# Performance work log

Measured on AMD Instinct MI355X. Metric: run time of the kernel, lower is better.

Reference implementation:

```python
import jax, jax.numpy as jnp
import numpy as np

N = 100000
E = 1600000
IN_DIM = 165
HID = 128
OUT_H = 64  # hidden_dim // 2

def setup_inputs() -> dict:
    key = jax.random.key(0)
    ks = jax.random.split(key, 8)
    x = jax.random.normal(ks[0], (N, IN_DIM), dtype=jnp.float32)
    edge_index = jax.random.randint(ks[1], (2, E), 0, N, dtype=jnp.int64)
    s1 = 1.0 / np.sqrt(IN_DIM)
    s2 = 1.0 / np.sqrt(HID)
    s3 = 1.0 / np.sqrt(OUT_H)
    return {
        "x": x,
        "edge_index": edge_index,
        "W1": jax.random.normal(ks[2], (IN_DIM, HID), dtype=jnp.float32) * s1,
        "b1": jnp.zeros((HID,), jnp.float32),
        "Wg": jax.random.normal(ks[3], (HID, OUT_H), dtype=jnp.float32) * s2,
        "a_src": jax.random.normal(ks[4], (OUT_H,), dtype=jnp.float32) * s3,
        "a_dst": jax.random.normal(ks[5], (OUT_H,), dtype=jnp.float32) * s3,
        "bg": jnp.zeros((OUT_H,), jnp.float32),
        "Wfc": jax.random.normal(ks[6], (OUT_H, 2), dtype=jnp.float32) * s3,
        "bfc": jnp.zeros((2,), jnp.float32),
    }

def _add_self_loops(edge_index, n):
    loops = jnp.arange(n, dtype=edge_index.dtype)
    row = jnp.concatenate([edge_index[0], loops])
    col = jnpp_concat = jnp.concatenate([edge_index[1], loops])
    return row, col

def _gcn_layer(x, row, col, W, b, n):
    deg = jax.ops.segment_sum(jnp.ones_like(col, dtype=x.dtype), col, num_segments=n)
    dinv = jnp.where(deg > 0, jax.lax.rsqrt(deg), 0.0)
    h = x @ W                                   # [N, HID]
    msg = h[row] * (dinv[row] * dinv[col])[:, None]  # [E+N, HID]
    return jax.ops.segment_sum(msg, col, num_segments=n) + b

def _gat_layer(x, row, col, W, a_src, a_dst, b, n):
    # single-head GATConv with self-loops, LeakyReLU(0.2), segment softmax over dst
    h = x @ W                                   # [N, OUT_H]
    e = jax.nn.leaky_relu((h @ a_src)[row] + (h @ a_dst)[col], negative_slope=0.2)
    m = jax.ops.segment_max(e, col, num_segments=n)
    ex = jnp.exp(e - m[col])
    s = jax.ops.segment_sum(ex, col, num_segments=n)
    alpha = ex / s[col]                         # every node has a self-loop => s > 0
    out = jax.ops.segment_sum(alpha[:, None] * h[row], col, num_segments=n)
    return out + b

def reference(x, edge_index, W1, b1, Wg, a_src, a_dst, bg, Wfc, bfc):
    n = x.shape[0]
    row, col = _add_self_loops(edge_index, n)
    h = jax.nn.relu(_gcn_layer(x, row, col, W1, b1, n))
    h = jax.nn.relu(_gat_layer(h, row, col, Wg, a_src, a_dst, bg, n))
    return h @ Wfc + bfc
```

## Files before the change

### kernel.cpp

```cpp
#include <hip/hip_runtime.h>
#include <math.h>

#define NSL 0.2f
#define IN_DIM 165
#define HID 128
#define OUT_H 64
#define NCB_MAX 512
#define EPB 4096

typedef __attribute__((ext_vector_type(8))) short bf16x8;
typedef __attribute__((ext_vector_type(4))) float f32x4;

__device__ inline unsigned pack_bf16(float a, float b) {
    unsigned ua = __float_as_uint(a);
    ua += 0x7FFFu + ((ua >> 16) & 1u);
    unsigned ub = __float_as_uint(b);
    ub += 0x7FFFu + ((ub >> 16) & 1u);
    return (ua >> 16) | (ub & 0xFFFF0000u);
}

__device__ __host__ inline int pcol(int i) {
    int j = i >> 1, odd = i & 1;
    return 32 * (j >> 4) + (j & 15) + 16 * odd;
}

__global__ __launch_bounds__(256) void chist(const int* __restrict__ coli, int E,
                                             int* __restrict__ ghist, int ncb) {
    __shared__ int h[NCB_MAX];
    for (int i = threadIdx.x; i < ncb; i += 256) h[i] = 0;
    __syncthreads();
    int e0 = blockIdx.x * EPB;
    int e1 = min(e0 + EPB, E);
    for (int e = e0 + threadIdx.x; e < e1; e += 256)
        atomicAdd(&h[coli[e] >> 8], 1);
    __syncthreads();
    for (int i = threadIdx.x; i < ncb; i += 256)
        if (h[i]) atomicAdd(&ghist[i], h[i]);
}

__global__ __launch_bounds__(NCB_MAX) void cscan(const int* __restrict__ ghist,
                                                 int* __restrict__ cstart,
                                                 int* __restrict__ gcursor,
                                                 int ncb, int E) {
    __shared__ int tmp[NCB_MAX];
    int tid = threadIdx.x;
    int v = (tid < ncb) ? ghist[tid] : 0;
    tmp[tid] = v;
    __syncthreads();
    for (int off = 1; off < NCB_MAX; off <<= 1) {
        int t = (tid >= off) ? tmp[tid - off] : 0;
        __syncthreads();
        tmp[tid] += t;
        __syncthreads();
    }
    if (tid < ncb) {
        int excl = tmp[tid] - v;
        cstart[tid] = excl;
        gcursor[tid] = excl;
    }
    if (tid == ncb - 1) cstart[ncb] = E;
}

__global__ __launch_bounds__(256) void pass1_scatter(const int* __restrict__ rowi,
                                                     const int* __restrict__ coli, int E,
                                                     int* __restrict__ gcursor,
                                                     unsigned* __restrict__ ebuf, int ncb) {
    __shared__ int hist[NCB_MAX];
    __shared__ int base[NCB_MAX];
    int e0 = blockIdx.x * EPB;
    int e1 = min(e0 + EPB, E);
    for (int i = threadIdx.x; i < ncb; i += 256) hist[i] = 0;
    __syncthreads();
    for (int e = e0 + threadIdx.x; e < e1; e += 256)
        atomicAdd(&hist[coli[e] >> 8], 1);
    __syncthreads();
    for (int i = threadIdx.x; i < ncb; i += 256) {
        int h = hist[i];
        base[i] = h ? atomicAdd(&gcursor[i], h) : 0;
        hist[i] = 0;
    }
    __syncthreads();
    for (int e = e0 + threadIdx.x; e < e1; e += 256) {
        int c = coli[e];
        int cb = c >> 8;
        int rank = atomicAdd(&hist[cb], 1);
        ebuf[base[cb] + rank] = ((unsigned)rowi[e] << 8) | (unsigned)(c & 255);
    }
}

__global__ __launch_bounds__(256) void pass2_all(const unsigned* __restrict__ ebuf,
                                                 const int* __restrict__ cstart,
                                                 int* __restrict__ offsets,
                                                 float* __restrict__ dinv,
                                                 int* __restrict__ csr_src,
                                                 int n, int E) {
    __shared__ int cnt[256];
    __shared__ int scan[256];
    __shared__ int offs[256];
    const int tid = threadIdx.x;
    const int cb = blockIdx.x;
    cnt[tid] = 0;
    __syncthreads();
    int s = cstart[cb], e1 = cstart[cb + 1];
    for (int e = s + tid; e < e1; e += 256)
        atomicAdd(&cnt[ebuf[e] & 255u], 1);
    __syncthreads();
    int v = cnt[tid];
    scan[tid] = v;
    __syncthreads();
#pragma unroll
    for (int off = 1; off < 256; off <<= 1) {
        int t = (tid >= off) ? scan[tid - off] : 0;
        __syncthreads();
        scan[tid] += t;
        __syncthreads();
    }
    int off0 = s + scan[tid] - v;
    offs[tid] = off0;
    int node = (cb << 8) + tid;
    if (node < n) {
        offsets[node] = off0;
        dinv[node] = rsqrtf((float)v + 1.0f);
    }
    if (cb == 0 && tid == 0) offsets[n] = E;
    cnt[tid] = 0;
    __syncthreads();
    for (int e = s + tid; e < e1; e += 256) {
        unsigned u = ebuf[e];
        int local = u & 255u;
        int rank = atomicAdd(&cnt[local], 1);
        csr_src[offs[local] + rank] = (int)(u >> 8);
    }
}

__global__ __launch_bounds__(256) void wprep_all(const float* __restrict__ W1,
                                                 const float* __restrict__ b1,
                                                 const float* __restrict__ Wg,
                                                 const float* __restrict__ bg,
                                                 const float* __restrict__ Wfc,
                                                 uint4* __restrict__ wfrag,
                                                 float* __restrict__ b1p,
                                                 uint4* __restrict__ wg2frag,
                                                 float* __restrict__ bgp,
                                                 float2* __restrict__ wfcp) {
    int idx = blockIdx.x * 256 + threadIdx.x;
    if (idx < 3072) {
        int q = idx & 3, n = (idx >> 2) & 127, c = idx >> 9;
        int k0 = c * 32 + q * 8;
        float f[8];
#pragma unroll
        for (int j = 0; j < 8; j++) {
            int k = k0 + j;
            f[j] = (k < IN_DIM) ? W1[k * 128 + n] : 0.f;
        }
        uint4 u;
        u.x = pack_bf16(f[0], f[1]);
        u.y = pack_bf16(f[2], f[3]);
        u.z = pack_bf16(f[4], f[5]);
        u.w = pack_bf16(f[6], f[7]);
        wfrag[idx] = u;
    } else if (idx < 4096) {
        int i2 = idx - 3072;
        int q = i2 & 3, n = (i2 >> 2) & 63, c = i2 >> 8;
        float f[8];
#pragma unroll
        for (int j = 0; j < 8; j++) {
            int ks = c * 32 + q * 8 + j;
            f[j] = Wg[pcol(ks) * 64 + n];
        }
        uint4 u;
        u.x = pack_bf16(f[0], f[1]);
        u.y = pack_bf16(f[2], f[3]);
        u.z = pack_bf16(f[4], f[5]);
        u.w = pack_bf16(f[6], f[7]);
        wg2frag[i2] = u;
    }
    if (idx < 128) b1p[idx] = b1[pcol(idx)];
    if (idx < 64) {
        int o = pcol(idx);
        bgp[idx] = bg[o];
        wfcp[idx] = make_float2(Wfc[o * 2], Wfc[o * 2 + 1]);
    }
}

__global__ __launch_bounds__(256) void gemm1_mfma(const float* __restrict__ x,
                                                  const uint4* __restrict__ wfrag,
                                                  const float* __restrict__ dinv,
                                                  unsigned char* __restrict__ h1p8,
                                                  float* __restrict__ h1s, int M) {
    const int t = threadIdx.x;
    const int wave = t >> 6;
    const int lane = t & 63;
    const int l16 = lane & 15;
    const int quad = lane >> 4;
    const int rowbase = blockIdx.x * 64 + wave * 16;

    int arow = rowbase + l16;
    if (arow >= M) arow = M - 1;
    const float* xr = x + (size_t)arow * IN_DIM;

    f32x4 acc[8];
#pragma unroll
    for (int nt = 0; nt < 8; nt++) acc[nt] = (f32x4){0.f, 0.f, 0.f, 0.f};

#pragma unroll
    for (int c = 0; c < 6; c++) {
        int k0 = c * 32 + quad * 8;
        float f[8];
#pragma unroll
        for (int j = 0; j < 8; j++)
            f[j] = (k0 + j < IN_DIM) ? xr[k0 + j] : 0.f;
        uint4 au;
        au.x = pack_bf16(f[0], f[1]);
        au.y = pack_bf16(f[2], f[3]);
        au.z = pack_bf16(f[4], f[5]);
        au.w = pack_bf16(f[6], f[7]);
        bf16x8 a = __builtin_bit_cast(bf16x8, au);
#pragma unroll
        for (int nt = 0; nt < 8; nt++) {
            uint4 bu = wfrag[(size_t)((c * 128 + nt * 16 + l16) * 4 + quad)];
            bf16x8 b = __builtin_bit_cast(bf16x8, bu);
            acc[nt] = __builtin_amdgcn_mfma_f32_16x16x32_bf16(a, b, acc[nt], 0, 0, 0);
        }
    }

#pragma unroll
    for (int r = 0; r < 4; r++) {
        int row = rowbase + quad * 4 + r;
        if (row < M) {
            float s = dinv[row];
            float v[8];
#pragma unroll
            for (int nt = 0; nt < 8; nt++) v[nt] = acc[nt][r] * s;
            float gm = fabsf(v[0]);
#pragma unroll
            for (int nt = 1; nt < 8; nt++) gm = fmaxf(gm, fabsf(v[nt]));
            gm = fmaxf(gm, __shfl_xor(gm, 1, 16));
            gm = fmaxf(gm, __shfl_xor(gm, 2, 16));
            gm = fmaxf(gm, __shfl_xor(gm, 4, 16));
            gm = fmaxf(gm, __shfl_xor(gm, 8, 16));
            float inv = gm > 0.f ? 127.0f / gm : 0.f;
            unsigned short* hr = (unsigned short*)(h1p8 + (size_t)row * 128);
#pragma unroll
            for (int p = 0; p < 4; p++) {
                int q0 = (int)rintf(v[2 * p] * inv);
                int q1 = (int)rintf(v[2 * p + 1] * inv);
                hr[p * 16 + l16] = (unsigned short)((q0 & 0xff) | ((q1 & 0xff) << 8));
            }
            if (l16 == 0) h1s[row] = gm * (1.0f / 127.0f);
        }
    }
}

__device__ inline void fma8i8(float* a, uint2 u, float s) {
    a[0] = fmaf((float)(char)(u.x), s, a[0]);
    a[1] = fmaf((float)(char)(u.x >> 8), s, a[1]);
    a[2] = fmaf((float)(char)(u.x >> 16), s, a[2]);
    a[3] = fmaf((float)(char)(u.x >> 24), s, a[3]);
    a[4] = fmaf((float)(char)(u.y), s, a[4]);
    a[5] = fmaf((float)(char)(u.y >> 8), s, a[5]);
    a[6] = fmaf((float)(char)(u.y >> 16), s, a[6]);
    a[7] = fmaf((float)(char)(u.y >> 24), s, a[7]);
}

__device__ inline void fma8(float* a, uint4 u, float w) {
    a[0] = fmaf(__uint_as_float(u.x << 16), w, a[0]);
    a[1] = fmaf(__uint_as_float(u.x & 0xFFFF0000u), w, a[1]);
    a[2] = fmaf(__uint_as_float(u.y << 16), w, a[2]);
    a[3] = fmaf(__uint_as_float(u.y & 0xFFFF0000u), w, a[3]);
    a[4] = fmaf(__uint_as_float(u.z << 16), w, a[4]);
    a[5] = fmaf(__uint_as_float(u.z & 0xFFFF0000u), w, a[5]);
    a[6] = fmaf(__uint_as_float(u.w << 16), w, a[6]);
    a[7] = fmaf(__uint_as_float(u.w & 0xFFFF0000u), w, a[7]);
}

__device__ inline float lexp(float e) {
    e = e > 0.f ? e : NSL * e;
    return __expf(e);
}

__global__ __launch_bounds__(256) void gcn_gather(const int* __restrict__ offsets,
                                                  const int* __restrict__ csr_src,
                                                  const uint2* __restrict__ h1v8,
                                                  const float* __restrict__ h1s,
                                                  const float* __restrict__ dinv,
                                                  const float* __restrict__ b1p,
                                                  uint4* __restrict__ gb, int n) {
    int node = (blockIdx.x * 256 + threadIdx.x) >> 4;
    int lane = threadIdx.x & 15;
    if (node >= n) return;
    int s0 = offsets[node], s1 = offsets[node + 1];

    float a0[8], a1[8], a2[8], a3[8];
#pragma unroll
    for (int i = 0; i < 8; i++) { a0[i] = 0.f; a1[i] = 0.f; a2[i] = 0.f; a3[i] = 0.f; }
    fma8i8(a0, h1v8[(size_t)node * 16 + lane], h1s[node]);

    int k = s0;
    if (s1 - k >= 8) {
        uint2 vA[8];
        float wA[8];
        {
            int r[8];
#pragma unroll
            for (int j = 0; j < 8; j++) r[j] = csr_src[k + j];
#pragma unroll
            for (int j = 0; j < 8; j++) vA[j] = h1v8[(size_t)r[j] * 16 + lane];
#pragma unroll
            for (int j = 0; j < 8; j++) wA[j] = h1s[r[j]];
        }
        k += 8;
        while (s1 - k >= 8) {
            uint2 vB[8];
            float wB[8];
            {
                int r[8];
#pragma unroll
                for (int j = 0; j < 8; j++) r[j] = csr_src[k + j];
#pragma unroll
                for (int j = 0; j < 8; j++) vB[j] = h1v8[(size_t)r[j] * 16 + lane];
#pragma unroll
                for (int j = 0; j < 8; j++) wB[j] = h1s[r[j]];
            }
            k += 8;
            fma8i8(a0, vA[0], wA[0]);
            fma8i8(a1, vA[1], wA[1]);
            fma8i8(a2, vA[2], wA[2]);
            fma8i8(a3, vA[3], wA[3]);
            fma8i8(a0, vA[4], wA[4]);
            fma8i8(a1, vA[5], wA[5]);
            fma8i8(a2, vA[6], wA[6]);
            fma8i8(a3, vA[7], wA[7]);
#pragma unroll
            for (int j = 0; j < 8; j++) { vA[j] = vB[j]; wA[j] = wB[j]; }
        }
        fma8i8(a0, vA[0], wA[0]);
        fma8i8(a1, vA[1], wA[1]);
        fma8i8(a2, vA[2], wA[2]);
        fma8i8(a3, vA[3], wA[3]);
        fma8i8(a0, vA[4], wA[4]);
        fma8i8(a1, vA[5], wA[5]);
        fma8i8(a2, vA[6], wA[6]);
        fma8i8(a3, vA[7], wA[7]);
    }
    int m = s1 - k;
    if (m > 0) {
        int r[8];
#pragma unroll
        for (int j = 0; j < 8; j++) r[j] = csr_src[j < m ? k + j : k];
        uint2 v[8];
#pragma unroll
        for (int j = 0; j < 8; j++) v[j] = h1v8[(size_t)r[j] * 16 + lane];
        float w[8];
#pragma unroll
        for (int j = 0; j < 8; j++) w[j] = (j < m) ? h1s[r[j]] : 0.f;
        fma8i8(a0, v[0], w[0]);
        fma8i8(a1, v[1], w[1]);
        fma8i8(a2, v[2], w[2]);
        fma8i8(a3, v[3], w[3]);
        fma8i8(a0, v[4], w[4]);
        fma8i8(a1, v[5], w[5]);
        fma8i8(a2, v[6], w[6]);
        fma8i8(a3, v[7], w[7]);
    }

    float dc = dinv[node];
    float4 bb0 = ((const float4*)b1p)[lane * 2];
    float4 bb1 = ((const float4*)b1p)[lane * 2 + 1];
    float o[8];
    o[0] = fmaxf(((a0[0] + a1[0]) + (a2[0] + a3[0])) * dc + bb0.x, 0.f);
    o[1] = fmaxf(((a0[1] + a1[1]) + (a2[1] + a3[1])) * dc + bb0.y, 0.f);
    o[2] = fmaxf(((a0[2] + a1[2]) + (a2[2] + a3[2])) * dc + bb0.z, 0.f);
    o[3] = fmaxf(((a0[3] + a1[3]) + (a2[3] + a3[3])) * dc + bb0.w, 0.f);
    o[4] = fmaxf(((a0[4] + a1[4]) + (a2[4] + a3[4])) * dc + bb1.x, 0.f);
    o[5] = fmaxf(((a0[5] + a1[5]) + (a2[5] + a3[5])) * dc + bb1.y, 0.f);
    o[6] = fmaxf(((a0[6] + a1[6]) + (a2[6] + a3[6])) * dc + bb1.z, 0.f);
    o[7] = fmaxf(((a0[7] + a1[7]) + (a2[7] + a3[7])) * dc + bb1.w, 0.f);
    uint4 pk;
    pk.x = pack_bf16(o[0], o[1]);
    pk.y = pack_bf16(o[2], o[3]);
    pk.z = pack_bf16(o[4], o[5]);
    pk.w = pack_bf16(o[6], o[7]);
    gb[(size_t)node * 16 + lane] = pk;
}

__global__ __launch_bounds__(256) void gemm2_mfma(const uint4* __restrict__ gb4,
                                                  const uint4* __restrict__ wg2frag,
                                                  const float* __restrict__ a_src,
                                                  const float* __restrict__ a_dst,
                                                  unsigned* __restrict__ h2b,
                                                  float* __restrict__ es,
                                                  float* __restrict__ ed, int M) {
    const int t = threadIdx.x;
    const int wave = t >> 6;
    const int lane = t & 63;
    const int l16 = lane & 15;
    const int quad = lane >> 4;
    const int rowbase = blockIdx.x * 64 + wave * 16;

    int arow = rowbase + l16;
    if (arow >= M) arow = M - 1;

    f32x4 acc[4];
#pragma unroll
    for (int nt = 0; nt < 4; nt++) acc[nt] = (f32x4){0.f, 0.f, 0.f, 0.f};

#pragma unroll
    for (int c = 0; c < 4; c++) {
        uint4 au = gb4[(size_t)arow * 16 + c * 4 + quad];
        bf16x8 a = __builtin_bit_cast(bf16x8, au);
#pragma unroll
        for (int nt = 0; nt < 4; nt++) {
            uint4 bu = wg2frag[(size_t)((c * 64 + nt * 16 + l16) * 4 + quad)];
            bf16x8 b = __builtin_bit_cast(bf16x8, bu);
            acc[nt] = __builtin_amdgcn_mfma_f32_16x16x32_bf16(a, b, acc[nt], 0, 0, 0);
        }
    }

    float as0 = a_src[l16], as1 = a_src[16 + l16], as2 = a_src[32 + l16], as3 = a_src[48 + l16];
    float ad0 = a_dst[l16], ad1 = a_dst[16 + l16], ad2 = a_dst[32 + l16], ad3 = a_dst[48 + l16];

#pragma unroll
    for (int r = 0; r < 4; r++) {
        int row = rowbase + quad * 4 + r;
        float ps = acc[0][r] * as0 + acc[1][r] * as1 + acc[2][r] * as2 + acc[3][r] * as3;
        float pd = acc[0][r] * ad0 + acc[1][r] * ad1 + acc[2][r] * ad2 + acc[3][r] * ad3;
#pragma unroll
        for (int m = 8; m; m >>= 1) {
            ps += __shfl_xor(ps, m, 16);
            pd += __shfl_xor(pd, m, 16);
        }
        if (row < M) {
            h2b[(size_t)row * 32 + l16]      = pack_bf16(acc[0][r], acc[1][r]);
            h2b[(size_t)row * 32 + 16 + l16] = pack_bf16(acc[2][r], acc[3][r]);
            if (l16 == 0) { es[row] = ps; ed[row] = pd; }
        }
    }
}

__global__ __launch_bounds__(256) void gat_fused(const int* __restrict__ offsets,
                                                 const int* __restrict__ csr_src,
                                                 const uint4* __restrict__ h2v,
                                                 const float* __restrict__ es,
                                                 const float* __restrict__ ed,
                                                 const float* __restrict__ bgp,
                                                 const float2* __restrict__ wfcp,
                                                 const float* __restrict__ bfc,
                                                 float* __restrict__ out, int n) {
    int node = (blockIdx.x * 256 + threadIdx.x) >> 3;
    int lane = threadIdx.x & 7;
    if (node >= n) return;
    int s0 = offsets[node], s1 = offsets[node + 1];
    float edc = ed[node];

    float x0s = lexp(es[node] + edc);
    float sA = x0s, sB = 0.f, sC = 0.f, sD = 0.f;
    float aA[8], aB[8], aC[8], aD[8];
#pragma unroll
    for (int i = 0; i < 8; i++) { aA[i] = 0.f; aB[i] = 0.f; aC[i] = 0.f; aD[i] = 0.f; }
    fma8(aA, h2v[(size_t)node * 8 + lane], x0s);

    int k = s0;
    if (s1 - k >= 4) {
        int r0 = csr_src[k], r1 = csr_src[k + 1], r2 = csr_src[k + 2], r3 = csr_src[k + 3];
        float e0 = es[r0], e1 = es[r1], e2 = es[r2], e3 = es[r3];
        uint4 v0 = h2v[(size_t)r0 * 8 + lane];
        uint4 v1 = h2v[(size_t)r1 * 8 + lane];
        uint4 v2 = h2v[(size_t)r2 * 8 + lane];
        uint4 v3 = h2v[(size_t)r3 * 8 + lane];
        k += 4;
        while (s1 - k >= 4) {
            int q0 = csr_src[k], q1 = csr_src[k + 1], q2 = csr_src[k + 2], q3 = csr_src[k + 3];
            float f0 = es[q0], f1 = es[q1], f2 = es[q2], f3 = es[q3];
            uint4 u0 = h2v[(size_t)q0 * 8 + lane];
            uint4 u1 = h2v[(size_t)q1 * 8 + lane];
            uint4 u2 = h2v[(size_t)q2 * 8 + lane];
            uint4 u3 = h2v[(size_t)q3 * 8 + lane];
            k += 4;
            float x0 = lexp(e0 + edc), x1 = lexp(e1 + edc);
            float x2 = lexp(e2 + edc), x3 = lexp(e3 + edc);
            sA += x0; sB += x1; sC += x2; sD += x3;
            fma8(aA, v0, x0);
            fma8(aB, v1, x1);
            fma8(aC, v2, x2);
            fma8(aD, v3, x3);
            e0 = f0; e1 = f1; e2 = f2; e3 = f3;
            v0 = u0; v1 = u1; v2 = u2; v3 = u3;
        }
        float x0 = lexp(e0 + edc), x1 = lexp(e1 + edc);
        float x2 = lexp(e2 + edc), x3 = lexp(e3 + edc);
        sA += x0; sB += x1; sC += x2; sD += x3;
        fma8(aA, v0, x0);
        fma8(aB, v1, x1);
        fma8(aC, v2, x2);
        fma8(aD, v3, x3);
    }
    for (; k < s1; k++) {
        int r = csr_src[k];
        float xv = lexp(es[r] + edc);
        sA += xv;
        fma8(aA, h2v[(size_t)r * 8 + lane], xv);
    }
    float s = (sA + sB) + (sC + sD);
    float rcp = 1.0f / s;
    float4 b0 = ((const float4*)bgp)[lane * 2];
    float4 b1 = ((const float4*)bgp)[lane * 2 + 1];
    float o[8];
    o[0] = fmaxf(((aA[0] + aB[0]) + (aC[0] + aD[0])) * rcp + b0.x, 0.f);
    o[1] = fmaxf(((aA[1] + aB[1]) + (aC[1] + aD[1])) * rcp + b0.y, 0.f);
    o[2] = fmaxf(((aA[2] + aB[2]) + (aC[2] + aD[2])) * rcp + b0.z, 0.f);
    o[3] = fmaxf(((aA[3] + aB[3]) + (aC[3] + aD[3])) * rcp + b0.w, 0.f);
    o[4] = fmaxf(((aA[4] + aB[4]) + (aC[4] + aD[4])) * rcp + b1.x, 0.f);
    o[5] = fmaxf(((aA[5] + aB[5]) + (aC[5] + aD[5])) * rcp + b1.y, 0.f);
    o[6] = fmaxf(((aA[6] + aB[6]) + (aC[6] + aD[6])) * rcp + b1.z, 0.f);
    o[7] = fmaxf(((aA[7] + aB[7]) + (aC[7] + aD[7])) * rcp + b1.w, 0.f);

    float p0 = 0.f, p1 = 0.f;
#pragma unroll
    for (int m2 = 0; m2 < 4; m2++) {
        float4 w = ((const float4*)wfcp)[lane * 4 + m2];
        p0 += o[2 * m2] * w.x + o[2 * m2 + 1] * w.z;
        p1 += o[2 * m2] * w.y + o[2 * m2 + 1] * w.w;
    }
#pragma unroll
    for (int m = 4; m; m >>= 1) {
        p0 += __shfl_xor(p0, m, 8);
        p1 += __shfl_xor(p1, m, 8);
    }
    if (lane == 0) {
        out[(size_t)node * 2 + 0] = p0 + bfc[0];
        out[(size_t)node * 2 + 1] = p1 + bfc[1];
    }
}

extern "C" void kernel_launch(void* const* d_in, const int* in_sizes, int n_in,
                              void* d_out, int out_size, void* d_ws, size_t ws_size,
                              hipStream_t stream) {
    const float* x     = (const float*)d_in[0];
    const int*   ei    = (const int*)d_in[1];
    const float* W1    = (const float*)d_in[2];
    const float* b1    = (const float*)d_in[3];
    const float* Wg    = (const float*)d_in[4];
    const float* a_src = (const float*)d_in[5];
    const float* a_dst = (const float*)d_in[6];
    const float* bg    = (const float*)d_in[7];
    const float* Wfc   = (const float*)d_in[8];
    const float* bfc   = (const float*)d_in[9];
    float* out = (float*)d_out;

    const int N = in_sizes[0] / IN_DIM;
    const int E = in_sizes[1] / 2;
    const int* rowi = ei;
    const int* coli = ei + E;
    const int ncb = (N + 255) >> 8;

    auto alignup = [](char* p) { return (char*)(((uintptr_t)p + 15) & ~(uintptr_t)15); };

    char* wsb = (char*)d_ws;
    int*   offsets = (int*)wsb;
    float* dinv    = (float*)(offsets + N + 8);
    float* es      = dinv + N;
    float* ed      = es + N;
    float* h1s     = ed + N;
    int*   ghist   = (int*)(h1s + N);
    int*   cstart  = ghist + NCB_MAX;
    int*   gcursor = cstart + NCB_MAX + 2;
    float* b1p     = (float*)(gcursor + NCB_MAX);
    float* bgp     = b1p + 128;
    float2* wfcp   = (float2*)(bgp + 64);
    uint4* wfrag   = (uint4*)alignup((char*)(wfcp + 64));
    uint4* wg2frag = wfrag + 3072;
    int*   csr_src = (int*)(wg2frag + 1024);
    unsigned* ebuf = (unsigned*)(csr_src + E);
    unsigned char* h1p8 = (unsigned char*)alignup((char*)(ebuf + E));
    uint4* gb      = (uint4*)alignup((char*)(h1p8 + (size_t)N * 128));
    unsigned* h2b  = (unsigned*)h1p8;

    hipMemsetAsync(ghist, 0, NCB_MAX * 4, stream);

    const int nbE = (E + EPB - 1) / EPB;

    chist<<<nbE, 256, 0, stream>>>(coli, E, ghist, ncb);
    cscan<<<1, NCB_MAX, 0, stream>>>(ghist, cstart, gcursor, ncb, E);
    pass1_scatter<<<nbE, 256, 0, stream>>>(rowi, coli, E, gcursor, ebuf, ncb);
    pass2_all<<<ncb, 256, 0, stream>>>(ebuf, cstart, offsets, dinv, csr_src, N, E);

    wprep_all<<<16, 256, 0, stream>>>(W1, b1, Wg, bg, Wfc, wfrag, b1p, wg2frag, bgp, wfcp);

    gemm1_mfma<<<(N + 63) / 64, 256, 0, stream>>>(x, wfrag, dinv, h1p8, h1s, N);

    gcn_gather<<<(N + 15) / 16, 256, 0, stream>>>(offsets, csr_src, (const uint2*)h1p8,
                                                  h1s, dinv, b1p, gb, N);

    gemm2_mfma<<<(N + 63) / 64, 256, 0, stream>>>(gb, wg2frag, a_src, a_dst, h2b, es, ed, N);

    gat_fused<<<(N + 31) / 32, 256, 0, stream>>>(offsets, csr_src, (const uint4*)h2b,
                                                 es, ed, bgp, wfcp, bfc, out, N);
}
```

Before: 324.3 us.

## Widen GAT gather to 16 lanes per node with 8-deep edge prefetch

After: 321.3 us. Within noise of the previous version (-0.9%).

```diff
diff --git a/kernel.cpp b/kernel.cpp
--- a/kernel.cpp
+++ b/kernel.cpp
@@ -263,15 +263,11 @@
     a[7] = fmaf((float)(char)(u.y >> 24), s, a[7]);
 }
 
-__device__ inline void fma8(float* a, uint4 u, float w) {
+__device__ inline void fma4(float* a, uint2 u, float w) {
     a[0] = fmaf(__uint_as_float(u.x << 16), w, a[0]);
     a[1] = fmaf(__uint_as_float(u.x & 0xFFFF0000u), w, a[1]);
     a[2] = fmaf(__uint_as_float(u.y << 16), w, a[2]);
     a[3] = fmaf(__uint_as_float(u.y & 0xFFFF0000u), w, a[3]);
-    a[4] = fmaf(__uint_as_float(u.z << 16), w, a[4]);
-    a[5] = fmaf(__uint_as_float(u.z & 0xFFFF0000u), w, a[5]);
-    a[6] = fmaf(__uint_as_float(u.w << 16), w, a[6]);
-    a[7] = fmaf(__uint_as_float(u.w & 0xFFFF0000u), w, a[7]);
 }
 
 __device__ inline float lexp(float e) {
@@ -440,92 +436,133 @@
 
 __global__ __launch_bounds__(256) void gat_fused(const int* __restrict__ offsets,
                                                  const int* __restrict__ csr_src,
-                                                 const uint4* __restrict__ h2v,
+                                                 const uint2* __restrict__ h2v,
                                                  const float* __restrict__ es,
                                                  const float* __restrict__ ed,
                                                  const float* __restrict__ bgp,
                                                  const float2* __restrict__ wfcp,
                                                  const float* __restrict__ bfc,
                                                  float* __restrict__ out, int n) {
-    int node = (blockIdx.x * 256 + threadIdx.x) >> 3;
-    int lane = threadIdx.x & 7;
+    int node = (blockIdx.x * 256 + threadIdx.x) >> 4;
+    int lane = threadIdx.x & 15;
     if (node >= n) return;
     int s0 = offsets[node], s1 = offsets[node + 1];
     float edc = ed[node];
 
     float x0s = lexp(es[node] + edc);
     float sA = x0s, sB = 0.f, sC = 0.f, sD = 0.f;
-    float aA[8], aB[8], aC[8], aD[8];
-#pragma unroll
-    for (int i = 0; i < 8; i++) { aA[i] = 0.f; aB[i] = 0.f; aC[i] = 0.f; aD[i] = 0.f; }
-    fma8(aA, h2v[(size_t)node * 8 + lane], x0s);
+    float aA[4], aB[4], aC[4], aD[4];
+#pragma unroll
+    for (int i = 0; i < 4; i++) { aA[i] = 0.f; aB[i] = 0.f; aC[i] = 0.f; aD[i] = 0.f; }
+    fma4(aA, h2v[(size_t)node * 16 + lane], x0s);
 
     int k = s0;
-    if (s1 - k >= 4) {
-        int r0 = csr_src[k], r1 = csr_src[k + 1], r2 = csr_src[k + 2], r3 = csr_src[k + 3];
-        float e0 = es[r0], e1 = es[r1], e2 = es[r2], e3 = es[r3];
-        uint4 v0 = h2v[(size_t)r0 * 8 + lane];
-        uint4 v1 = h2v[(size_t)r1 * 8 + lane];
-        uint4 v2 = h2v[(size_t)r2 * 8 + lane];
-        uint4 v3 = h2v[(size_t)r3 * 8 + lane];
-        k += 4;
-        while (s1 - k >= 4) {
-            int q0 = csr_src[k], q1 = csr_src[k + 1], q2 = csr_src[k + 2], q3 = csr_src[k + 3];
-            float f0 = es[q0], f1 = es[q1], f2 = es[q2], f3 = es[q3];
-            uint4 u0 = h2v[(size_t)q0 * 8 + lane];
-            uint4 u1 = h2v[(size_t)q1 * 8 + lane];
-            uint4 u2 = h2v[(size_t)q2 * 8 + lane];
-            uint4 u3 = h2v[(size_t)q3 * 8 + lane];
-            k += 4;
-            float x0 = lexp(e0 + edc), x1 = lexp(e1 + edc);
-            float x2 = lexp(e2 + edc), x3 = lexp(e3 + edc);
+    if (s1 - k >= 8) {
+        uint2 vA[8];
+        float eA[8];
+        {
+            int r[8];
+#pragma unroll
+            for (int j = 0; j < 8; j++) r[j] = csr_src[k + j];
+#pragma unroll
+            for (int j = 0; j < 8; j++) vA[j] = h2v[(size_t)r[j] * 16 + lane];
+#pragma unroll
+            for (int j = 0; j < 8; j++) eA[j] = es[r[j]];
+        }
+        k += 8;
+        while (s1 - k >= 8) {
+            uint2 vB[8];
+            float eB[8];
+            {
+                int r[8];
+#pragma unroll
+                for (int j = 0; j < 8; j++) r[j] = csr_src[k + j];
+#pragma unroll
+                for (int j = 0; j < 8; j++) vB[j] = h2v[(size_t)r[j] * 16 + lane];
+#pragma unroll
+                for (int j = 0; j < 8; j++) eB[j] = es[r[j]];
+            }
+            k += 8;
+            float x0 = lexp(eA[0] + edc), x1 = lexp(eA[1] + edc);
+            float x2 = lexp(eA[2] + edc), x3 = lexp(eA[3] + edc);
+            float x4 = lexp(eA[4] + edc), x5 = lexp(eA[5] + edc);
+            float x6 = lexp(eA[6] + edc), x7 = lexp(eA[7] + edc);
             sA += x0; sB += x1; sC += x2; sD += x3;
-            fma8(aA, v0, x0);
-            fma8(aB, v1, x1);
-            fma8(aC, v2, x2);
-            fma8(aD, v3, x3);
-            e0 = f0; e1 = f1; e2 = f2; e3 = f3;
-            v0 = u0; v1 = u1; v2 = u2; v3 = u3;
-        }
-        float x0 = lexp(e0 + edc), x1 = lexp(e1 + edc);
-        float x2 = lexp(e2 + edc), x3 = lexp(e3 + edc);
+            sA += x4; sB += x5; sC += x6; sD += x7;
+            fma4(aA, vA[0], x0);
+            fma4(aB, vA[1], x1);
+            fma4(aC, vA[2], x2);
+            fma4(aD, vA[3], x3);
+            fma4(aA, vA[4], x4);
+            fma4(aB, vA[5], x5);
+            fma4(aC, vA[6], x6);
+            fma4(aD, vA[7], x7);
+#pragma unroll
+            for (int j = 0; j < 8; j++) { vA[j] = vB[j]; eA[j] = eB[j]; }
+        }
+        float x0 = lexp(eA[0] + edc), x1 = lexp(eA[1] + edc);
+        float x2 = lexp(eA[2] + edc), x3 = lexp(eA[3] + edc);
+        float x4 = lexp(eA[4] + edc), x5 = lexp(eA[5] + edc);
+        float x6 = lexp(eA[6] + edc), x7 = lexp(eA[7] + edc);
         sA += x0; sB += x1; sC += x2; sD += x3;
-        fma8(aA, v0, x0);
-        fma8(aB, v1, x1);
-        fma8(aC, v2, x2);
-        fma8(aD, v3, x3);
-    }
-    for (; k < s1; k++) {
-        int r = csr_src[k];
-        float xv = lexp(es[r] + edc);
-        sA += xv;
-        fma8(aA, h2v[(size_t)r * 8 + lane], xv);
-    }
+        sA += x4; sB += x5; sC += x6; sD += x7;
+        fma4(aA, vA[0], x0);
+        fma4(aB, vA[1], x1);
+        fma4(aC, vA[2], x2);
+        fma4(aD, vA[3], x3);
+        fma4(aA, vA[4], x4);
+        fma4(aB, vA[5], x5);
+        fma4(aC, vA[6], x6);
+        fma4(aD, vA[7], x7);
+    }
+    int m = s1 - k;
+    if (m > 0) {
+        int r[8];
+#pragma unroll
+        for (int j = 0; j < 8; j++) r[j] = csr_src[j < m ? k + j : k];
+        uint2 v[8];
+#pragma unroll
+        for (int j = 0; j < 8; j++) v[j] = h2v[(size_t)r[j] * 16 + lane];
+        float ev[8];
+#pragma unroll
+        for (int j = 0; j < 8; j++) ev[j] = es[r[j]];
+        float x0 = (0 < m) ? lexp(ev[0] + edc) : 0.f;
+        float x1 = (1 < m) ? lexp(ev[1] + edc) : 0.f;
+        float x2 = (2 < m) ? lexp(ev[2] + edc) : 0.f;
+        float x3 = (3 < m) ? lexp(ev[3] + edc) : 0.f;
+        float x4 = (4 < m) ? lexp(ev[4] + edc) : 0.f;
+        float x5 = (5 < m) ? lexp(ev[5] + edc) : 0.f;
+        float x6 = (6 < m) ? lexp(ev[6] + edc) : 0.f;
+        float x7 = (7 < m) ? lexp(ev[7] + edc) : 0.f;
+        sA += x0; sB += x1; sC += x2; sD += x3;
+        sA += x4; sB += x5; sC += x6; sD += x7;
+        fma4(aA, v[0], x0);
+        fma4(aB, v[1], x1);
+        fma4(aC, v[2], x2);
+        fma4(aD, v[3], x3);
+        fma4(aA, v[4], x4);
+        fma4(aB, v[5], x5);
+        fma4(aC, v[6], x6);
+        fma4(aD, v[7], x7);
+    }
+
     float s = (sA + sB) + (sC + sD);
     float rcp = 1.0f / s;
-    float4 b0 = ((const float4*)bgp)[lane * 2];
-    float4 b1 = ((const float4*)bgp)[lane * 2 + 1];
-    float o[8];
-    o[0] = fmaxf(((aA[0] + aB[0]) + (aC[0] + aD[0])) * rcp + b0.x, 0.f);
-    o[1] = fmaxf(((aA[1] + aB[1]) + (aC[1] + aD[1])) * rcp + b0.y, 0.f);
-    o[2] = fmaxf(((aA[2] + aB[2]) + (aC[2] + aD[2])) * rcp + b0.z, 0.f);
-    o[3] = fmaxf(((aA[3] + aB[3]) + (aC[3] + aD[3])) * rcp + b0.w, 0.f);
-    o[4] = fmaxf(((aA[4] + aB[4]) + (aC[4] + aD[4])) * rcp + b1.x, 0.f);
-    o[5] = fmaxf(((aA[5] + aB[5]) + (aC[5] + aD[5])) * rcp + b1.y, 0.f);
-    o[6] = fmaxf(((aA[6] + aB[6]) + (aC[6] + aD[6])) * rcp + b1.z, 0.f);
-    o[7] = fmaxf(((aA[7] + aB[7]) + (aC[7] + aD[7])) * rcp + b1.w, 0.f);
-
-    float p0 = 0.f, p1 = 0.f;
-#pragma unroll
-    for (int m2 = 0; m2 < 4; m2++) {
-        float4 w = ((const float4*)wfcp)[lane * 4 + m2];
-        p0 += o[2 * m2] * w.x + o[2 * m2 + 1] * w.z;
-        p1 += o[2 * m2] * w.y + o[2 * m2 + 1] * w.w;
-    }
-#pragma unroll
-    for (int m = 4; m; m >>= 1) {
-        p0 += __shfl_xor(p0, m, 8);
-        p1 += __shfl_xor(p1, m, 8);
+    float4 bb = ((const float4*)bgp)[lane];
+    float o[4];
+    o[0] = fmaxf(((aA[0] + aB[0]) + (aC[0] + aD[0])) * rcp + bb.x, 0.f);
+    o[1] = fmaxf(((aA[1] + aB[1]) + (aC[1] + aD[1])) * rcp + bb.y, 0.f);
+    o[2] = fmaxf(((aA[2] + aB[2]) + (aC[2] + aD[2])) * rcp + bb.z, 0.f);
+    o[3] = fmaxf(((aA[3] + aB[3]) + (aC[3] + aD[3])) * rcp + bb.w, 0.f);
+
+    float4 w01 = ((const float4*)wfcp)[lane * 2];
+    float4 w23 = ((const float4*)wfcp)[lane * 2 + 1];
+    float p0 = o[0] * w01.x + o[1] * w01.z + o[2] * w23.x + o[3] * w23.z;
+    float p1 = o[0] * w01.y + o[1] * w01.w + o[2] * w23.y + o[3] * w23.w;
+#pragma unroll
+    for (int mm = 8; mm; mm >>= 1) {
+        p0 += __shfl_xor(p0, mm, 16);
+        p1 += __shfl_xor(p1, mm, 16);
     }
     if (lane == 0) {
         out[(size_t)node * 2 + 0] = p0 + bfc[0];
@@ -594,6 +631,6 @@
 
     gemm2_mfma<<<(N + 63) / 64, 256, 0, stream>>>(gb, wg2frag, a_src, a_dst, h2b, es, ed, N);
 
-    gat_fused<<<(N + 31) / 32, 256, 0, stream>>>(offsets, csr_src, (const uint4*)h2b,
+    gat_fused<<<(N + 15) / 16, 256, 0, stream>>>(offsets, csr_src, (const uint2*)h2b,
                                                  es, ed, bgp, wfcp, bfc, out, N);
 }
```
